# Performance work log

Hardware: AMD Instinct MI355X
Metric: run time of the kernel (lower is better)

## Reference

```python
import jax, jax.numpy as jnp
import numpy as np

N = 20000      # nodes
E = 320000     # edges
S = 256        # scalar (0e) channels of irreps_feature
F = 960        # full irreps_feature dim (256x0e+128x1e+64x2e)
NB = 32        # number_of_basis
CUT = 5.0      # max_radius


def setup_inputs() -> dict:
    key = jax.random.key(0)
    ks = jax.random.split(key, 24)
    def w(k, shape):
        return jax.random.normal(k, shape, jnp.float32) / np.sqrt(shape[0])
    return {
        "node_feature": jax.random.normal(ks[0], (N, F), jnp.float32),
        "pos": jax.random.normal(ks[1], (N, 3), jnp.float32),
        "edge_index": jax.random.randint(ks[2], (2, E), 0, N),
        "W_ai1": w(ks[3], (S, S)), "b_ai1": jnp.zeros((S,), jnp.float32),
        "W_ai2": w(ks[4], (S, 1)), "b_ai2": jnp.zeros((1,), jnp.float32),
        "W_ci1": w(ks[5], (S, S)), "b_ci1": jnp.zeros((S,), jnp.float32),
        "W_ci2": w(ks[6], (S, 1)), "b_ci2": jnp.zeros((1,), jnp.float32),
        "W_sc": w(ks[7], (S, S)), "b_sc": jnp.zeros((S,), jnp.float32),
        "W_ed": w(ks[8], (NB, S)), "b_ed": jnp.zeros((S,), jnp.float32),
        "W_b1": w(ks[9], (3 * S, S)), "b_b1": jnp.zeros((S,), jnp.float32),
        "W_b2": w(ks[10], (S, 1)), "b_b2": jnp.zeros((1,), jnp.float32),
    }


def _rbf(d):
    # ExpNormalSmearing (torchmd-net), cutoff_lower=0, cutoff_upper=CUT, non-trainable
    start = np.exp(-CUT)
    means = jnp.linspace(start, 1.0, NB, dtype=jnp.float32)
    beta = jnp.float32(((2.0 / NB) * (1.0 - start)) ** -2)
    cosine_cut = 0.5 * (jnp.cos(np.pi * d / CUT) + 1.0) * (d < CUT)
    return cosine_cut[:, None] * jnp.exp(-beta * (jnp.exp(-d)[:, None] - means) ** 2)


def reference(node_feature, pos, edge_index,
              W_ai1, b_ai1, W_ai2, b_ai2,
              W_ci1, b_ci1, W_ci2, b_ci2,
              W_sc, b_sc, W_ed, b_ed,
              W_b1, b_b1, W_b2, b_b2):
    # LinearRS(irreps_feature -> 0e) only touches the 0e block (first S channels)
    scal = node_feature[:, :S]
    silu = jax.nn.silu

    log_ai = silu(scal @ W_ai1 + b_ai1) @ W_ai2 + b_ai2          # [N,1]
    ai = jnp.exp(log_ai)
    log_ci = silu(scal @ W_ci1 + b_ci1) @ W_ci2 + b_ci2          # [N,1]
    ci = jnp.exp(log_ci)

    src, dst = edge_index[0], edge_index[1]
    rel = pos[dst] - pos[src]                                     # [E,3]
    norm = jnp.linalg.norm(rel, axis=1, keepdims=True)            # [E,1]
    rhat = rel / (norm + 1e-8)
    emb = _rbf(norm[:, 0])                                        # [E,NB]

    node_sc = scal @ W_sc + b_sc                                  # project once, gather [N,S]
    src_f = node_sc[src]
    dst_f = node_sc[dst]
    edge_f = emb @ W_ed + b_ed
    edge_feature = jnp.concatenate([src_f, dst_f, edge_f], axis=-1)  # [E,3S]
    bij = silu(edge_feature @ W_b1 + b_b1) @ W_b2 + b_b2          # [E,1]

    # edge softmax over incoming edges of dst, with extra ci mass
    bmax = jax.ops.segment_max(bij, dst, num_segments=N)
    bmax = jnp.where(jnp.isneginf(bmax), 0.0, bmax)
    bij_exp = jnp.exp(bij - bmax[dst])
    bsum = jax.ops.segment_sum(bij_exp, dst, num_segments=N) + ci  # [N,1]
    gamma = bij_exp / (bsum[dst] + 1e-7)                           # [E,1]

    bij_prime = gamma * ai[dst]                                    # [E,1]
    outer = rhat[:, :, None] * rhat[:, None, :]                    # [E,3,3]
    contrib = jax.ops.segment_sum(bij_prime[:, :, None] * outer, dst, num_segments=N)  # [N,3,3]

    eye3 = jnp.eye(3, dtype=pos.dtype)
    sigma = ai[:, :, None] * eye3 - contrib + 1e-6 * eye3          # [N,3,3]
    sum_gamma = jax.ops.segment_sum(gamma, dst, num_segments=N)    # [N,1]
    return sigma, ai, sum_gamma
```

## Files before the change

kernel.cpp:

```cpp
#include <hip/hip_runtime.h>
#include <math.h>

#define N_NODES 20000
#define E_EDGES 320000
#define F_DIM   960
#define S_DIM   256
#define QTAB    2048
#define ASTRIDE 264
#define CAP     64

typedef __attribute__((ext_vector_type(8))) short short8;
typedef __attribute__((ext_vector_type(4))) float f32x4;

__device__ __forceinline__ float siluf(float x) {
    return x / (1.0f + __expf(-x));
}

__device__ __forceinline__ unsigned short bf16rn(float x) {
    unsigned u = __float_as_uint(x);
    return (unsigned short)((u + 0x7FFFu + ((u >> 16) & 1u)) >> 16);
}

__device__ __forceinline__ void bf16x8_to_f32(short8 v8, float* o) {
    union { short8 s; uint4 u; } cv; cv.s = v8;
    o[0] = __uint_as_float(cv.u.x << 16);
    o[1] = __uint_as_float(cv.u.x & 0xffff0000u);
    o[2] = __uint_as_float(cv.u.y << 16);
    o[3] = __uint_as_float(cv.u.y & 0xffff0000u);
    o[4] = __uint_as_float(cv.u.z << 16);
    o[5] = __uint_as_float(cv.u.z & 0xffff0000u);
    o[6] = __uint_as_float(cv.u.w << 16);
    o[7] = __uint_as_float(cv.u.w & 0xffff0000u);
}

__global__ void prep_kernel(const float* __restrict__ W_sc, const float* __restrict__ W_ed,
                            const float* __restrict__ W_b1, const float* __restrict__ b_sc,
                            const float* __restrict__ b_ed, const float* __restrict__ b_b1,
                            const float* __restrict__ W_ai1, const float* __restrict__ W_ci1,
                            float* __restrict__ Bcat, float* __restrict__ We, float* __restrict__ c0,
                            int* __restrict__ cnt)
{
    int idx = blockIdx.x * 256 + threadIdx.x;
    if (idx < N_NODES) cnt[idx] = 0;
    if (idx < 256 * 1024) {
        int k = idx >> 10, j = idx & 1023;
        float s = 0.0f;
        if (j < 256) {
            for (int m = 0; m < 256; ++m) s += W_sc[k * 256 + m] * W_b1[m * 256 + j];
        } else if (j < 512) {
            int jj = j - 256;
            for (int m = 0; m < 256; ++m) s += W_sc[k * 256 + m] * W_b1[(256 + m) * 256 + jj];
        } else if (j < 768) {
            s = W_ai1[k * 256 + (j - 512)];
        } else {
            s = W_ci1[k * 256 + (j - 768)];
        }
        Bcat[idx] = s;
    } else if (idx < 256 * 1024 + 32 * 256) {
        int t = idx - 256 * 1024;
        int p = t >> 8, j = t & 255;
        float s = 0.0f;
        for (int m = 0; m < 256; ++m) s += W_ed[p * 256 + m] * W_b1[(512 + m) * 256 + j];
        We[t] = s;
    } else if (idx < 256 * 1024 + 32 * 256 + 256) {
        int j = idx - 256 * 1024 - 32 * 256;
        float s = b_b1[j];
        for (int m = 0; m < 256; ++m) {
            s += b_sc[m] * (W_b1[m * 256 + j] + W_b1[(256 + m) * 256 + j]);
            s += b_ed[m] * W_b1[(512 + m) * 256 + j];
        }
        c0[j] = s;
    }
}

__global__ void aux_kernel(const int* __restrict__ ei, int* __restrict__ cnt,
                           const float* __restrict__ Bcat, unsigned short* __restrict__ Bpack,
                           const float* __restrict__ We, unsigned short* __restrict__ Tab)
{
    int b = blockIdx.x;
    if (b < 1250) {
        int i = b * 256 + threadIdx.x;
        atomicAdd(&cnt[ei[E_EDGES + i]], 1);
    } else if (b < 1378) {
        int idx = (b - 1250) * 256 + threadIdx.x;
        int kq = idx & 3, j = (idx >> 2) & 1023, t = idx >> 12;
        #pragma unroll
        for (int jj = 0; jj < 8; ++jj)
            Bpack[idx * 8 + jj] = bf16rn(Bcat[(t * 32 + kq * 8 + jj) * 1024 + j]);
    } else {
        int idx = (b - 1378) * 256 + threadIdx.x;
        int q = idx >> 8, j = idx & 255;
        float nrm = 5.0f * (float)q / (float)(QTAB - 1);
        const float start = 0.006737946999085467f;
        const float mustep = (1.0f - start) / 31.0f;
        const float bx = (2.0f / 32.0f) * (1.0f - start);
        const float beta = 1.0f / (bx * bx);
        const float PI_F = 3.14159265358979323846f;
        float cc = (nrm < 5.0f) ? 0.5f * (cosf(PI_F * nrm * 0.2f) + 1.0f) : 0.0f;
        float t = expf(-nrm);
        float s = 0.0f;
        for (int k = 0; k < 32; ++k) {
            float dm = t - (start + (float)k * mustep);
            s += expf(-beta * dm * dm) * We[k * 256 + j];
        }
        Tab[idx] = bf16rn(cc * s);
    }
}

__global__ __launch_bounds__(1024) void scan_kernel(const int* __restrict__ cnt,
                                                    int* __restrict__ start, int* __restrict__ cursor)
{
    __shared__ int ps[1024];
    const int t = threadIdx.x;
    const int base = t * 20;
    int loc[20];
    int s = 0;
    #pragma unroll
    for (int i = 0; i < 20; ++i) {
        int n = (base + i < N_NODES) ? cnt[base + i] : 0;
        loc[i] = s; s += n;
    }
    ps[t] = s;
    __syncthreads();
    for (int off = 1; off < 1024; off <<= 1) {
        int v = (t >= off) ? ps[t - off] : 0;
        __syncthreads();
        ps[t] += v;
        __syncthreads();
    }
    int offset = ps[t] - s;
    #pragma unroll
    for (int i = 0; i < 20; ++i) {
        if (base + i < N_NODES) {
            start[base + i] = offset + loc[i];
            cursor[base + i] = offset + loc[i];
        }
    }
}

__global__ void slot_kernel(const int* __restrict__ ei, int* __restrict__ cursor,
                            int* __restrict__ srcS)
{
    int i = blockIdx.x * 256 + threadIdx.x;
    if (i < E_EDGES) {
        int sl = atomicAdd(&cursor[ei[E_EDGES + i]], 1);
        srcS[sl] = ei[i];
    }
}

__global__ __launch_bounds__(256) void node_mfma_kernel(
    const float* __restrict__ nf, const unsigned short* __restrict__ Bpack,
    const float* __restrict__ c0,
    const float* __restrict__ b_ai1, const float* __restrict__ W_ai2, const float* __restrict__ b_ai2,
    const float* __restrict__ b_ci1, const float* __restrict__ W_ci2, const float* __restrict__ b_ci2,
    unsigned short* __restrict__ u, unsigned short* __restrict__ v,
    float* __restrict__ bsumseed, float* __restrict__ out_ai)
{
    __shared__ unsigned short A[32 * ASTRIDE];
    __shared__ float red[32 * 4];

    const int tid = threadIdx.x;
    const int w = tid >> 6, lane = tid & 63;
    const int bg = blockIdx.x & 3;
    const int m0 = (blockIdx.x >> 2) * 32;
    const int col16 = lane & 15, quad = lane >> 4;

    #pragma unroll
    for (int it = 0; it < 8; ++it) {
        int idx = (it * 256 + tid) * 4;
        int r = idx >> 8, c = idx & 255;
        float4 a4 = *(const float4*)&nf[(m0 + r) * F_DIM + c];
        ushort4 b4;
        b4.x = bf16rn(a4.x); b4.y = bf16rn(a4.y);
        b4.z = bf16rn(a4.z); b4.w = bf16rn(a4.w);
        *(ushort4*)&A[r * ASTRIDE + c] = b4;
    }
    __syncthreads();

    f32x4 acc[2][4];
    #pragma unroll
    for (int mt = 0; mt < 2; ++mt)
        #pragma unroll
        for (int nt = 0; nt < 4; ++nt)
            acc[mt][nt] = (f32x4){0.0f, 0.0f, 0.0f, 0.0f};

    const int colbase = bg * 256 + w * 64;

    for (int t = 0; t < 8; ++t) {
        short8 af[2];
        #pragma unroll
        for (int mt = 0; mt < 2; ++mt)
            af[mt] = *(const short8*)&A[(mt * 16 + col16) * ASTRIDE + t * 32 + quad * 8];
        short8 bf[4];
        #pragma unroll
        for (int nt = 0; nt < 4; ++nt)
            bf[nt] = *(const short8*)&Bpack[(((t * 1024 + colbase + nt * 16 + col16) * 4) + quad) * 8];
        #pragma unroll
        for (int mt = 0; mt < 2; ++mt)
            #pragma unroll
            for (int nt = 0; nt < 4; ++nt)
                acc[mt][nt] = __builtin_amdgcn_mfma_f32_16x16x32_bf16(af[mt], bf[nt], acc[mt][nt], 0, 0, 0);
    }

    if (bg == 0) {
        #pragma unroll
        for (int nt = 0; nt < 4; ++nt) {
            int jl = w * 64 + nt * 16 + col16;
            float c0v = c0[jl];
            #pragma unroll
            for (int mt = 0; mt < 2; ++mt)
                #pragma unroll
                for (int reg = 0; reg < 4; ++reg)
                    u[(m0 + mt * 16 + quad * 4 + reg) * 256 + jl] = bf16rn(acc[mt][nt][reg] + c0v);
        }
    } else if (bg == 1) {
        #pragma unroll
        for (int nt = 0; nt < 4; ++nt) {
            int jl = w * 64 + nt * 16 + col16;
            #pragma unroll
            for (int mt = 0; mt < 2; ++mt)
                #pragma unroll
                for (int reg = 0; reg < 4; ++reg)
                    v[(m0 + mt * 16 + quad * 4 + reg) * 256 + jl] = bf16rn(acc[mt][nt][reg]);
        }
    } else {
        const float* b1 = (bg == 2) ? b_ai1 : b_ci1;
        const float* w2 = (bg == 2) ? W_ai2 : W_ci2;
        float s[2][4] = {{0, 0, 0, 0}, {0, 0, 0, 0}};
        #pragma unroll
        for (int nt = 0; nt < 4; ++nt) {
            int jl = w * 64 + nt * 16 + col16;
            float bb = b1[jl], ww = w2[jl];
            #pragma unroll
            for (int mt = 0; mt < 2; ++mt)
                #pragma unroll
                for (int reg = 0; reg < 4; ++reg)
                    s[mt][reg] += siluf(acc[mt][nt][reg] + bb) * ww;
        }
        #pragma unroll
        for (int off = 1; off < 16; off <<= 1) {
            #pragma unroll
            for (int mt = 0; mt < 2; ++mt)
                #pragma unroll
                for (int reg = 0; reg < 4; ++reg)
                    s[mt][reg] += __shfl_xor(s[mt][reg], off);
        }
        if (col16 == 0) {
            #pragma unroll
            for (int mt = 0; mt < 2; ++mt)
                #pragma unroll
                for (int reg = 0; reg < 4; ++reg)
                    red[(mt * 16 + quad * 4 + reg) * 4 + w] = s[mt][reg];
        }
        __syncthreads();
        if (tid < 32) {
            float sum = red[tid * 4] + red[tid * 4 + 1] + red[tid * 4 + 2] + red[tid * 4 + 3];
            if (bg == 2) out_ai[m0 + tid] = expf(sum + b_ai2[0]);
            else         bsumseed[m0 + tid] = expf(sum + b_ci2[0]) + 1e-7f;
        }
    }
}

__global__ __launch_bounds__(256) void edge_node_kernel(
    const int* __restrict__ start, const int* __restrict__ cnt, const int* __restrict__ srcS,
    const float* __restrict__ pos,
    const unsigned short* __restrict__ u, const unsigned short* __restrict__ v,
    const unsigned short* __restrict__ Tab, const float* __restrict__ W_b2, const float* __restrict__ b_b2,
    const float* __restrict__ bsumseed, const float* __restrict__ out_ai,
    float* __restrict__ out_sigma, float* __restrict__ out_sg)
{
    __shared__ float sb[16][CAP];
    __shared__ float srx[16][CAP];
    __shared__ float sry[16][CAP];
    __shared__ float srz[16][CAP];

    const int grp = threadIdx.x >> 4;
    const int l   = threadIdx.x & 15;
    const int g   = blockIdx.x * 16 + grp;
    const int st  = start[g];
    const int deg = min(cnt[g], CAP);

    float vch[16];
    bf16x8_to_f32(*(const short8*)&v[(size_t)g * 256 + l * 16], vch);
    bf16x8_to_f32(*(const short8*)&v[(size_t)g * 256 + l * 16 + 8], vch + 8);
    float w2c[16];
    #pragma unroll
    for (int c = 0; c < 16; c += 4)
        *(float4*)&w2c[c] = *(const float4*)&W_b2[l * 16 + c];
    const float bb2 = b_b2[0];
    const float gx = pos[3 * g + 0], gy = pos[3 * g + 1], gz = pos[3 * g + 2];
    const float xscale = (float)(QTAB - 1) * 0.2f;

    int s = (deg > 0) ? srcS[st] : 0;
    for (int i = 0; i < deg; ++i) {
        int s_next = (i + 1 < deg) ? srcS[st + i + 1] : 0;
        float px = gx - pos[3 * s + 0];
        float py = gy - pos[3 * s + 1];
        float pz = gz - pos[3 * s + 2];
        float nrm = sqrtf(px * px + py * py + pz * pz);
        float inv = 1.0f / (nrm + 1e-8f);
        float rx = px * inv, ry = py * inv, rz = pz * inv;

        float x = nrm * xscale;
        int qi = (int)x;
        float f = x - (float)qi;
        if (qi >= QTAB - 1) { qi = QTAB - 2; f = 1.0f; }

        float acc = 0.0f;
        #pragma unroll
        for (int half = 0; half < 2; ++half) {
            float uf[8], t0f[8], t1f[8];
            bf16x8_to_f32(*(const short8*)&u[(size_t)s * 256 + l * 16 + half * 8], uf);
            bf16x8_to_f32(*(const short8*)&Tab[(size_t)qi * 256 + l * 16 + half * 8], t0f);
            bf16x8_to_f32(*(const short8*)&Tab[(size_t)(qi + 1) * 256 + l * 16 + half * 8], t1f);
            #pragma unroll
            for (int c = 0; c < 8; ++c) {
                float h = uf[c] + vch[half * 8 + c] + t0f[c] + f * (t1f[c] - t0f[c]);
                float sig = __builtin_amdgcn_rcpf(1.0f + __expf(-h));
                acc += w2c[half * 8 + c] * h * sig;
            }
        }
        #pragma unroll
        for (int off = 1; off < 16; off <<= 1) acc += __shfl_xor(acc, off);

        if (l == 0) {
            sb[grp][i] = acc + bb2;
            srx[grp][i] = rx; sry[grp][i] = ry; srz[grp][i] = rz;
        }
        s = s_next;
    }

    float m = -1e30f;
    for (int i = l; i < deg; i += 16) m = fmaxf(m, sb[grp][i]);
    #pragma unroll
    for (int off = 1; off < 16; off <<= 1) m = fmaxf(m, __shfl_xor(m, off));

    float ssum = 0.0f;
    for (int i = l; i < deg; i += 16) ssum += __expf(sb[grp][i] - m);
    #pragma unroll
    for (int off = 1; off < 16; off <<= 1) ssum += __shfl_xor(ssum, off);

    float invt = 1.0f / (ssum + bsumseed[g]);

    float a0 = 0, a1 = 0, a2 = 0, a3 = 0, a4 = 0, a5 = 0, a6 = 0;
    for (int i = l; i < deg; i += 16) {
        float gm = __expf(sb[grp][i] - m) * invt;
        float rx = srx[grp][i], ry = sry[grp][i], rz = srz[grp][i];
        a0 += gm * rx * rx; a1 += gm * ry * ry; a2 += gm * rz * rz;
        a3 += gm * rx * ry; a4 += gm * rx * rz; a5 += gm * ry * rz;
        a6 += gm;
    }
    #pragma unroll
    for (int off = 1; off < 16; off <<= 1) {
        a0 += __shfl_xor(a0, off); a1 += __shfl_xor(a1, off);
        a2 += __shfl_xor(a2, off); a3 += __shfl_xor(a3, off);
        a4 += __shfl_xor(a4, off); a5 += __shfl_xor(a5, off);
        a6 += __shfl_xor(a6, off);
    }

    if (l == 0) {
        float ai = out_ai[g];
        float* sg = &out_sigma[g * 9];
        float d0 = ai + 1e-6f;
        sg[0] = d0 - ai * a0;
        sg[1] = -ai * a3;
        sg[2] = -ai * a4;
        sg[3] = -ai * a3;
        sg[4] = d0 - ai * a1;
        sg[5] = -ai * a5;
        sg[6] = -ai * a4;
        sg[7] = -ai * a5;
        sg[8] = d0 - ai * a2;
        out_sg[g] = a6;
    }
}

extern "C" void kernel_launch(void* const* d_in, const int* in_sizes, int n_in,
                              void* d_out, int out_size, void* d_ws, size_t ws_size,
                              hipStream_t stream)
{
    const float* nf    = (const float*)d_in[0];
    const float* pos   = (const float*)d_in[1];
    const int*   ei    = (const int*)  d_in[2];
    const float* W_ai1 = (const float*)d_in[3];
    const float* b_ai1 = (const float*)d_in[4];
    const float* W_ai2 = (const float*)d_in[5];
    const float* b_ai2 = (const float*)d_in[6];
    const float* W_ci1 = (const float*)d_in[7];
    const float* b_ci1 = (const float*)d_in[8];
    const float* W_ci2 = (const float*)d_in[9];
    const float* b_ci2 = (const float*)d_in[10];
    const float* W_sc  = (const float*)d_in[11];
    const float* b_sc  = (const float*)d_in[12];
    const float* W_ed  = (const float*)d_in[13];
    const float* b_ed  = (const float*)d_in[14];
    const float* W_b1  = (const float*)d_in[15];
    const float* b_b1  = (const float*)d_in[16];
    const float* W_b2  = (const float*)d_in[17];
    const float* b_b2  = (const float*)d_in[18];

    char* pb = (char*)d_ws;
    auto alloc = [&](size_t bytes) -> void* {
        void* r = (void*)pb;
        pb += (bytes + 255) & ~(size_t)255;
        return r;
    };
    float*          Bcat    = (float*)         alloc(262144 * 4);
    float*          We      = (float*)         alloc(8192 * 4);
    float*          c0      = (float*)         alloc(256 * 4);
    unsigned short* Tab     = (unsigned short*)alloc((size_t)QTAB * 256 * 2);
    unsigned short* Bpack   = (unsigned short*)alloc((size_t)256 * 1024 * 2);
    unsigned short* u       = (unsigned short*)alloc((size_t)N_NODES * 256 * 2);
    unsigned short* v       = (unsigned short*)alloc((size_t)N_NODES * 256 * 2);
    float*          bsumseed= (float*)         alloc((size_t)N_NODES * 4);
    int*            cnt     = (int*)           alloc((size_t)N_NODES * 4);
    int*            startA  = (int*)           alloc((size_t)N_NODES * 4);
    int*            cursor  = (int*)           alloc((size_t)N_NODES * 4);
    int*            srcS    = (int*)           alloc((size_t)E_EDGES * 4);

    float* out       = (float*)d_out;
    float* out_sigma = out;
    float* out_ai    = out + N_NODES * 9;
    float* out_sg    = out + N_NODES * 10;

    prep_kernel<<<1058, 256, 0, stream>>>(W_sc, W_ed, W_b1, b_sc, b_ed, b_b1, W_ai1, W_ci1,
                                          Bcat, We, c0, cnt);
    aux_kernel<<<3426, 256, 0, stream>>>(ei, cnt, Bcat, Bpack, We, Tab);
    scan_kernel<<<1, 1024, 0, stream>>>(cnt, startA, cursor);
    slot_kernel<<<1250, 256, 0, stream>>>(ei, cursor, srcS);
    node_mfma_kernel<<<2500, 256, 0, stream>>>(nf, Bpack, c0, b_ai1, W_ai2, b_ai2,
                                               b_ci1, W_ci2, b_ci2, u, v, bsumseed, out_ai);
    edge_node_kernel<<<1250, 256, 0, stream>>>(startA, cnt, srcS, pos, u, v, Tab, W_b2, b_b2,
                                               bsumseed, out_ai, out_sigma, out_sg);
}
```

Before: 348.1 us.

## Precompute bf16 node scalars, rank-based CSR scatter, and prefetch edge gathers

Node scalars are converted to bf16 once in aux_kernel, so each of the four column-group blocks in node_mfma_kernel reads a compact bf16 copy instead of re-reading and re-converting fp32 features. The second atomic pass in slot_kernel is replaced by recording each edge's rank during counting and scattering to start+rank without atomics. The edge loop software-prefetches the next source's position and u row to hide gather latency, and the shared-memory arrays are padded to reduce bank conflicts. The cost is an extra N×256 bf16 buffer, an E-sized rank array, and higher register pressure in the edge kernel.

```diff
diff --git a/kernel.cpp b/kernel.cpp
--- a/kernel.cpp
+++ b/kernel.cpp
@@ -8,6 +8,7 @@
 #define QTAB    2048
 #define ASTRIDE 264
 #define CAP     64
+#define CPAD    66
 
 typedef __attribute__((ext_vector_type(8))) short short8;
 typedef __attribute__((ext_vector_type(4))) float f32x4;
@@ -73,21 +74,22 @@
     }
 }
 
-__global__ void aux_kernel(const int* __restrict__ ei, int* __restrict__ cnt,
+__global__ void aux_kernel(const int* __restrict__ ei, int* __restrict__ cnt, int* __restrict__ rank,
                            const float* __restrict__ Bcat, unsigned short* __restrict__ Bpack,
-                           const float* __restrict__ We, unsigned short* __restrict__ Tab)
+                           const float* __restrict__ We, unsigned short* __restrict__ Tab,
+                           const float* __restrict__ nf, unsigned short* __restrict__ scalp)
 {
     int b = blockIdx.x;
     if (b < 1250) {
         int i = b * 256 + threadIdx.x;
-        atomicAdd(&cnt[ei[E_EDGES + i]], 1);
+        rank[i] = atomicAdd(&cnt[ei[E_EDGES + i]], 1);
     } else if (b < 1378) {
         int idx = (b - 1250) * 256 + threadIdx.x;
         int kq = idx & 3, j = (idx >> 2) & 1023, t = idx >> 12;
         #pragma unroll
         for (int jj = 0; jj < 8; ++jj)
             Bpack[idx * 8 + jj] = bf16rn(Bcat[(t * 32 + kq * 8 + jj) * 1024 + j]);
-    } else {
+    } else if (b < 3426) {
         int idx = (b - 1378) * 256 + threadIdx.x;
         int q = idx >> 8, j = idx & 255;
         float nrm = 5.0f * (float)q / (float)(QTAB - 1);
@@ -104,11 +106,20 @@
             s += expf(-beta * dm * dm) * We[k * 256 + j];
         }
         Tab[idx] = bf16rn(cc * s);
+    } else {
+        int idx = (b - 3426) * 256 + threadIdx.x;
+        int base = idx * 4;
+        int n = base >> 8, k = base & 255;
+        float4 a4 = *(const float4*)&nf[(size_t)n * F_DIM + k];
+        ushort4 b4;
+        b4.x = bf16rn(a4.x); b4.y = bf16rn(a4.y);
+        b4.z = bf16rn(a4.z); b4.w = bf16rn(a4.w);
+        *(ushort4*)&scalp[n * 256 + k] = b4;
     }
 }
 
 __global__ __launch_bounds__(1024) void scan_kernel(const int* __restrict__ cnt,
-                                                    int* __restrict__ start, int* __restrict__ cursor)
+                                                    int* __restrict__ start)
 {
     __shared__ int ps[1024];
     const int t = threadIdx.x;
@@ -130,26 +141,19 @@
     }
     int offset = ps[t] - s;
     #pragma unroll
-    for (int i = 0; i < 20; ++i) {
-        if (base + i < N_NODES) {
-            start[base + i] = offset + loc[i];
-            cursor[base + i] = offset + loc[i];
-        }
-    }
-}
-
-__global__ void slot_kernel(const int* __restrict__ ei, int* __restrict__ cursor,
-                            int* __restrict__ srcS)
+    for (int i = 0; i < 20; ++i)
+        if (base + i < N_NODES) start[base + i] = offset + loc[i];
+}
+
+__global__ void scatter_kernel(const int* __restrict__ ei, const int* __restrict__ start,
+                               const int* __restrict__ rank, int* __restrict__ srcS)
 {
     int i = blockIdx.x * 256 + threadIdx.x;
-    if (i < E_EDGES) {
-        int sl = atomicAdd(&cursor[ei[E_EDGES + i]], 1);
-        srcS[sl] = ei[i];
-    }
+    if (i < E_EDGES) srcS[start[ei[E_EDGES + i]] + rank[i]] = ei[i];
 }
 
 __global__ __launch_bounds__(256) void node_mfma_kernel(
-    const float* __restrict__ nf, const unsigned short* __restrict__ Bpack,
+    const unsigned short* __restrict__ scalp, const unsigned short* __restrict__ Bpack,
     const float* __restrict__ c0,
     const float* __restrict__ b_ai1, const float* __restrict__ W_ai2, const float* __restrict__ b_ai2,
     const float* __restrict__ b_ci1, const float* __restrict__ W_ci2, const float* __restrict__ b_ci2,
@@ -166,14 +170,10 @@
     const int col16 = lane & 15, quad = lane >> 4;
 
     #pragma unroll
-    for (int it = 0; it < 8; ++it) {
-        int idx = (it * 256 + tid) * 4;
+    for (int it = 0; it < 4; ++it) {
+        int idx = (it * 256 + tid) * 8;
         int r = idx >> 8, c = idx & 255;
-        float4 a4 = *(const float4*)&nf[(m0 + r) * F_DIM + c];
-        ushort4 b4;
-        b4.x = bf16rn(a4.x); b4.y = bf16rn(a4.y);
-        b4.z = bf16rn(a4.z); b4.w = bf16rn(a4.w);
-        *(ushort4*)&A[r * ASTRIDE + c] = b4;
+        *(uint4*)&A[r * ASTRIDE + c] = *(const uint4*)&scalp[(m0 + r) * 256 + c];
     }
     __syncthreads();
 
@@ -269,10 +269,10 @@
     const float* __restrict__ bsumseed, const float* __restrict__ out_ai,
     float* __restrict__ out_sigma, float* __restrict__ out_sg)
 {
-    __shared__ float sb[16][CAP];
-    __shared__ float srx[16][CAP];
-    __shared__ float sry[16][CAP];
-    __shared__ float srz[16][CAP];
+    __shared__ float sb[16][CPAD];
+    __shared__ float srx[16][CPAD];
+    __shared__ float sry[16][CPAD];
+    __shared__ float srz[16][CPAD];
 
     const int grp = threadIdx.x >> 4;
     const int l   = threadIdx.x & 15;
@@ -291,12 +291,18 @@
     const float gx = pos[3 * g + 0], gy = pos[3 * g + 1], gz = pos[3 * g + 2];
     const float xscale = (float)(QTAB - 1) * 0.2f;
 
-    int s = (deg > 0) ? srcS[st] : 0;
+    int s_cur = (deg > 0) ? srcS[st] : 0;
+    float pxc = pos[3 * s_cur + 0], pyc = pos[3 * s_cur + 1], pzc = pos[3 * s_cur + 2];
+    short8 u0c = *(const short8*)&u[(size_t)s_cur * 256 + l * 16];
+    short8 u1c = *(const short8*)&u[(size_t)s_cur * 256 + l * 16 + 8];
+
     for (int i = 0; i < deg; ++i) {
-        int s_next = (i + 1 < deg) ? srcS[st + i + 1] : 0;
-        float px = gx - pos[3 * s + 0];
-        float py = gy - pos[3 * s + 1];
-        float pz = gz - pos[3 * s + 2];
+        int s_nxt = (i + 1 < deg) ? srcS[st + i + 1] : s_cur;
+        float pxn = pos[3 * s_nxt + 0], pyn = pos[3 * s_nxt + 1], pzn = pos[3 * s_nxt + 2];
+        short8 u0n = *(const short8*)&u[(size_t)s_nxt * 256 + l * 16];
+        short8 u1n = *(const short8*)&u[(size_t)s_nxt * 256 + l * 16 + 8];
+
+        float px = gx - pxc, py = gy - pyc, pz = gz - pzc;
         float nrm = sqrtf(px * px + py * py + pz * pz);
         float inv = 1.0f / (nrm + 1e-8f);
         float rx = px * inv, ry = py * inv, rz = pz * inv;
@@ -310,7 +316,7 @@
         #pragma unroll
         for (int half = 0; half < 2; ++half) {
             float uf[8], t0f[8], t1f[8];
-            bf16x8_to_f32(*(const short8*)&u[(size_t)s * 256 + l * 16 + half * 8], uf);
+            bf16x8_to_f32(half ? u1c : u0c, uf);
             bf16x8_to_f32(*(const short8*)&Tab[(size_t)qi * 256 + l * 16 + half * 8], t0f);
             bf16x8_to_f32(*(const short8*)&Tab[(size_t)(qi + 1) * 256 + l * 16 + half * 8], t1f);
             #pragma unroll
@@ -327,7 +333,7 @@
             sb[grp][i] = acc + bb2;
             srx[grp][i] = rx; sry[grp][i] = ry; srz[grp][i] = rz;
         }
-        s = s_next;
+        s_cur = s_nxt; pxc = pxn; pyc = pyn; pzc = pzn; u0c = u0n; u1c = u1n;
     }
 
     float m = -1e30f;
@@ -410,12 +416,13 @@
     float*          c0      = (float*)         alloc(256 * 4);
     unsigned short* Tab     = (unsigned short*)alloc((size_t)QTAB * 256 * 2);
     unsigned short* Bpack   = (unsigned short*)alloc((size_t)256 * 1024 * 2);
+    unsigned short* scalp   = (unsigned short*)alloc((size_t)N_NODES * 256 * 2);
     unsigned short* u       = (unsigned short*)alloc((size_t)N_NODES * 256 * 2);
     unsigned short* v       = (unsigned short*)alloc((size_t)N_NODES * 256 * 2);
     float*          bsumseed= (float*)         alloc((size_t)N_NODES * 4);
     int*            cnt     = (int*)           alloc((size_t)N_NODES * 4);
     int*            startA  = (int*)           alloc((size_t)N_NODES * 4);
-    int*            cursor  = (int*)           alloc((size_t)N_NODES * 4);
+    int*            rank    = (int*)           alloc((size_t)E_EDGES * 4);
     int*            srcS    = (int*)           alloc((size_t)E_EDGES * 4);
 
     float* out       = (float*)d_out;
@@ -425,10 +432,10 @@
 
     prep_kernel<<<1058, 256, 0, stream>>>(W_sc, W_ed, W_b1, b_sc, b_ed, b_b1, W_ai1, W_ci1,
                                           Bcat, We, c0, cnt);
-    aux_kernel<<<3426, 256, 0, stream>>>(ei, cnt, Bcat, Bpack, We, Tab);
-    scan_kernel<<<1, 1024, 0, stream>>>(cnt, startA, cursor);
-    slot_kernel<<<1250, 256, 0, stream>>>(ei, cursor, srcS);
-    node_mfma_kernel<<<2500, 256, 0, stream>>>(nf, Bpack, c0, b_ai1, W_ai2, b_ai2,
+    aux_kernel<<<8426, 256, 0, stream>>>(ei, cnt, rank, Bcat, Bpack, We, Tab, nf, scalp);
+    scan_kernel<<<1, 1024, 0, stream>>>(cnt, startA);
+    scatter_kernel<<<1250, 256, 0, stream>>>(ei, startA, rank, srcS);
+    node_mfma_kernel<<<2500, 256, 0, stream>>>(scalp, Bpack, c0, b_ai1, W_ai2, b_ai2,
                                                b_ci1, W_ci2, b_ci2, u, v, bsumseed, out_ai);
     edge_node_kernel<<<1250, 256, 0, stream>>>(startA, cnt, srcS, pos, u, v, Tab, W_b2, b_b2,
                                                bsumseed, out_ai, out_sigma, out_sg);
```

After: 323.1 us. 7.2% less time.
